# Optimization experiments

Measured on AMD Instinct MI355X. Metric: run time of the kernel, lower is better.

Reference implementation:

```python
import jax, jax.numpy as jnp
import numpy as np

D_MODEL = 2048
NUM_HEADS = 16
HEAD_DIM = D_MODEL // NUM_HEADS
D_FF = 4 * D_MODEL
B, L = 2, 2048
LN_EPS = 1e-6


def layer_norm(x, scale, bias):
    x32 = x.astype(jnp.float32)
    mu = jnp.mean(x32, axis=-1, keepdims=True)
    var = jnp.mean(jnp.square(x32 - mu), axis=-1, keepdims=True)
    return (x32 - mu) * jax.lax.rsqrt(var + LN_EPS) * scale + bias


def setup_inputs() -> dict:
    key = jax.random.key(0)
    ks = jax.random.split(key, 10)
    s = 1.0 / np.sqrt(D_MODEL)
    x = jax.random.normal(ks[0], (B, L, D_MODEL), dtype=jnp.float32)
    mask = jnp.tril(jnp.ones((L, L), dtype=bool))[None, None, :, :]  # causal [1,1,L,L]
    wq = jax.random.normal(ks[1], (D_MODEL, D_MODEL), jnp.float32) * s
    wk = jax.random.normal(ks[2], (D_MODEL, D_MODEL), jnp.float32) * s
    wv = jax.random.normal(ks[3], (D_MODEL, D_MODEL), jnp.float32) * s
    wo = jax.random.normal(ks[4], (D_MODEL, D_MODEL), jnp.float32) * s
    w1 = jax.random.normal(ks[5], (D_MODEL, D_FF), jnp.float32) * s
    b1 = jnp.zeros((D_FF,), jnp.float32)
    w2 = jax.random.normal(ks[6], (D_FF, D_MODEL), jnp.float32) * (1.0 / np.sqrt(D_FF))
    b2 = jnp.zeros((D_MODEL,), jnp.float32)
    ln1_scale = jnp.ones((D_MODEL,), jnp.float32)
    ln1_bias = jnp.zeros((D_MODEL,), jnp.float32)
    ln2_scale = jnp.ones((D_MODEL,), jnp.float32)
    ln2_bias = jnp.zeros((D_MODEL,), jnp.float32)
    return {"x": x, "mask": mask, "ln1_scale": ln1_scale, "ln1_bias": ln1_bias,
            "wq": wq, "wk": wk, "wv": wv, "wo": wo,
            "ln2_scale": ln2_scale, "ln2_bias": ln2_bias,
            "w1": w1, "b1": b1, "w2": w2, "b2": b2}


def reference(x, mask, ln1_scale, ln1_bias, wq, wk, wv, wo,
              ln2_scale, ln2_bias, w1, b1, w2, b2):
    residual = x
    h = layer_norm(x, ln1_scale, ln1_bias)
    b, l, _ = h.shape
    q = (h @ wq).reshape(b, l, NUM_HEADS, HEAD_DIM)
    k = (h @ wk).reshape(b, l, NUM_HEADS, HEAD_DIM)
    v = (h @ wv).reshape(b, l, NUM_HEADS, HEAD_DIM)
    scores = jnp.einsum('bqhd,bkhd->bhqk', q, k) / jnp.sqrt(jnp.float32(HEAD_DIM))
    scores = jnp.where(mask, scores, -100000.0)
    attn = jax.nn.softmax(scores, axis=-1)
    attn_out = jnp.einsum('bhqk,bkhd->bqhd', attn, v).reshape(b, l, D_MODEL)
    x = residual + attn_out @ wo
    mlp = jax.nn.gelu(layer_norm(x, ln2_scale, ln2_bias) @ w1 + b1)
    return x + mlp @ w2 + b2
```

## Files before the change

kernel.cpp:

```cpp
#include <hip/hip_runtime.h>
#include <hip/hip_bf16.h>

typedef unsigned short u16;
typedef __bf16 bf16x8 __attribute__((ext_vector_type(8)));
typedef float f32x4 __attribute__((ext_vector_type(4)));

#define D_MODEL 2048
#define D_FF    8192
#define NH      16
#define HD      128
#define BATCH   2
#define SEQ     2048
#define ROWS    (BATCH*SEQ)

__device__ __forceinline__ u16 f2bf(float f) {
  union { __hip_bfloat16 h; u16 u; } cv;
  cv.h = __float2bfloat16(f);
  return cv.u;
}

__device__ __forceinline__ void gload16(const u16* g, u16* l) {
  __builtin_amdgcn_global_load_lds((const __attribute__((address_space(1))) void*)g,
                                   (__attribute__((address_space(3))) void*)l,
                                   16, 0, 0);
}

__device__ __forceinline__ float gelu_f(float x) {
  const float k0 = 0.7978845608028654f, k1 = 0.044715f;
  return 0.5f * x * (1.0f + tanhf(k0 * (x + k1 * x * x * x)));
}

__global__ __launch_bounds__(256) void ln_bf16_kernel(
    const float* __restrict__ x, const float* __restrict__ sc,
    const float* __restrict__ bs, u16* __restrict__ out)
{
  __shared__ float red[8];
  const int row = blockIdx.x, t = threadIdx.x;
  const int w = t >> 6, l = t & 63;
  const float* xr = x + (size_t)row * D_MODEL;
  float4 a = ((const float4*)xr)[t*2];
  float4 b = ((const float4*)xr)[t*2+1];
  float s  = a.x+a.y+a.z+a.w + b.x+b.y+b.z+b.w;
  float s2 = a.x*a.x+a.y*a.y+a.z*a.z+a.w*a.w + b.x*b.x+b.y*b.y+b.z*b.z+b.w*b.w;
  for (int off = 32; off; off >>= 1) { s += __shfl_down(s, off); s2 += __shfl_down(s2, off); }
  if (l == 0) { red[w] = s; red[4+w] = s2; }
  __syncthreads();
  s  = red[0]+red[1]+red[2]+red[3];
  s2 = red[4]+red[5]+red[6]+red[7];
  const float mu  = s * (1.0f / D_MODEL);
  const float var = s2 * (1.0f / D_MODEL) - mu * mu;
  const float inv = rsqrtf(var + 1e-6f);
  float4 g0 = ((const float4*)sc)[t*2], g1 = ((const float4*)sc)[t*2+1];
  float4 q0 = ((const float4*)bs)[t*2], q1 = ((const float4*)bs)[t*2+1];
  union { u16 u[8]; uint4 v; } o;
  o.u[0] = f2bf((a.x-mu)*inv*g0.x + q0.x);
  o.u[1] = f2bf((a.y-mu)*inv*g0.y + q0.y);
  o.u[2] = f2bf((a.z-mu)*inv*g0.z + q0.z);
  o.u[3] = f2bf((a.w-mu)*inv*g0.w + q0.w);
  o.u[4] = f2bf((b.x-mu)*inv*g1.x + q1.x);
  o.u[5] = f2bf((b.y-mu)*inv*g1.y + q1.y);
  o.u[6] = f2bf((b.z-mu)*inv*g1.z + q1.z);
  o.u[7] = f2bf((b.w-mu)*inv*g1.w + q1.w);
  *(uint4*)(&out[(size_t)row * D_MODEL + t*8]) = o.v;
}

__global__ __launch_bounds__(256) void transpose_w(
    const float* __restrict__ in, u16* __restrict__ out, int R, int C)
{
  __shared__ float tile[32][33];
  const int t = threadIdx.x;
  const int c0 = blockIdx.x*32, r0 = blockIdx.y*32;
  const int col = t & 31, rb = t >> 5;
#pragma unroll
  for (int i = 0; i < 4; ++i)
    tile[rb + i*8][col] = in[(size_t)(r0 + rb + i*8)*C + c0 + col];
  __syncthreads();
#pragma unroll
  for (int i = 0; i < 4; ++i)
    out[(size_t)(c0 + rb + i*8)*R + r0 + col] = f2bf(tile[col][rb + i*8]);
}

__global__ __launch_bounds__(256) void transpose_v(
    const u16* __restrict__ qkv, u16* __restrict__ vt)
{
  __shared__ u16 tile[32][34];
  const int t = threadIdx.x;
  const int b = blockIdx.z;
  const int c0 = blockIdx.x*32, r0 = blockIdx.y*32;
  const int col = t & 31, rb = t >> 5;
  const u16* inb = qkv + (size_t)b*SEQ*3*D_MODEL + 2*D_MODEL;
#pragma unroll
  for (int i = 0; i < 4; ++i)
    tile[rb+i*8][col] = inb[(size_t)(r0+rb+i*8)*(3*D_MODEL) + c0+col];
  __syncthreads();
  u16* ob = vt + (size_t)b*SEQ*D_MODEL;
#pragma unroll
  for (int i = 0; i < 4; ++i)
    ob[(size_t)(c0+rb+i*8)*SEQ + r0+col] = tile[col][rb+i*8];
}

template<int EPI, int BNP>
__global__ __launch_bounds__(512, 1) void gemm8p(
    const u16* __restrict__ A, const u16* __restrict__ BT,
    void* __restrict__ Cout, const float* __restrict__ bias,
    const float* __restrict__ res, int N, int K, int gridN)
{
  constexpr int GB    = BNP / 128;
  constexpr int MF    = (BNP == 256) ? 8 : 4;
  constexpr int BHALF = BNP * 32;
  constexpr int BUFU  = 16384 + BNP * 64;
  __shared__ __align__(16) u16 lds[2 * BUFU];
  const int t = threadIdx.x;
  const int nwg = gridDim.x;
  const int wg = (int)blockIdx.x;
  const int wgid = (wg & 7) * (nwg >> 3) + (wg >> 3);
  const int bx = wgid % gridN, by = wgid / gridN;
  const int m0 = by * 256, n0 = bx * BNP;
  const int w = t >> 6, l = t & 63;
  const int wm = (BNP == 256) ? (w >> 2) : (w >> 1);
  const int wn = (BNP == 256) ? (w & 3) : (w & 1);
  const int l15 = l & 15, lq = l >> 4;

  const int srow = t >> 2;
  const int c0s  = (t & 3) ^ ((srow >> 1) & 3);
  const u16* aS0 = A  + (size_t)(m0 + srow) * K + c0s * 8;
  const u16* aS1 = A  + (size_t)(m0 + 128 + srow) * K + c0s * 8;
  const u16* bS0 = BT + (size_t)(n0 + srow) * K + c0s * 8;
  const u16* bS1 = BT + (size_t)(n0 + (GB == 2 ? 128 : 0) + srow) * K + c0s * 8;

  int offA_[MF], offB_[4];
#pragma unroll
  for (int i = 0; i < MF; ++i) {
    const int ra = wm * (MF * 16) + i * 16 + l15;
    offA_[i] = ra * 32 + ((lq ^ ((ra >> 1) & 3)) * 8);
  }
#pragma unroll
  for (int j = 0; j < 4; ++j) {
    const int rb = wn * 64 + j * 16 + l15;
    offB_[j] = rb * 32 + ((lq ^ ((rb >> 1) & 3)) * 8);
  }

  f32x4 acc[MF][4] = {};
  const int nt = K >> 6;

#define STAGE(dst, Tn, kh) { \
    gload16(aS0 + (size_t)(Tn)*64 + (kh)*32, (dst) + (kh)*8192 + t*8); \
    gload16(aS1 + (size_t)(Tn)*64 + (kh)*32, (dst) + (kh)*8192 + 4096 + t*8); \
    gload16(bS0 + (size_t)(Tn)*64 + (kh)*32, (dst) + 16384 + (kh)*BHALF + t*8); \
    if (GB == 2) gload16(bS1 + (size_t)(Tn)*64 + (kh)*32, (dst) + 16384 + (kh)*BHALF + 4096 + t*8); }
#define VMS { if (GB == 2) { asm volatile("s_waitcnt vmcnt(4)" ::: "memory"); } \
              else        { asm volatile("s_waitcnt vmcnt(3)" ::: "memory"); } \
              __builtin_amdgcn_sched_barrier(0); }
#define VM0 { asm volatile("s_waitcnt vmcnt(0)" ::: "memory"); __builtin_amdgcn_sched_barrier(0); }
#define NOP { }

#define PHASE(bufc, KH, STAGECODE, WAITCODE) { \
    bf16x8 af_[MF], bfv[4]; \
    _Pragma("unroll") \
    for (int i = 0; i < MF; ++i) \
      af_[i] = *(const bf16x8*)&(bufc)[offA_[i] + (KH)*8192]; \
    _Pragma("unroll") \
    for (int j = 0; j < 4; ++j) \
      bfv[j] = *(const bf16x8*)&(bufc)[offB_[j] + 16384 + (KH)*BHALF]; \
    STAGECODE; \
    __builtin_amdgcn_s_barrier(); \
    asm volatile("s_waitcnt lgkmcnt(0)" ::: "memory"); \
    __builtin_amdgcn_sched_barrier(0); \
    __builtin_amdgcn_s_setprio(1); \
    _Pragma("unroll") \
    for (int i = 0; i < MF; ++i) \
      _Pragma("unroll") \
      for (int j = 0; j < 4; ++j) \
        acc[i][j] = __builtin_amdgcn_mfma_f32_16x16x32_bf16(af_[i], bfv[j], acc[i][j], 0, 0, 0); \
    __builtin_amdgcn_s_setprio(0); \
    WAITCODE; \
    __builtin_amdgcn_s_barrier(); }

  STAGE(lds, 0, 0); STAGE(lds, 0, 1);
  VMS;
  __builtin_amdgcn_s_barrier();

  for (int T = 0; T < nt - 1; ++T) {
    u16* bufc = &lds[(T & 1) * BUFU];
    u16* bufn = &lds[((T + 1) & 1) * BUFU];
    PHASE(bufc, 0, STAGE(bufn, T + 1, 0), VMS);
    PHASE(bufc, 1, STAGE(bufn, T + 1, 1), VMS);
  }
  {
    u16* bufc = &lds[((nt - 1) & 1) * BUFU];
    PHASE(bufc, 0, NOP, VM0);
    PHASE(bufc, 1, NOP, NOP);
  }
#undef PHASE
#undef STAGE
#undef VMS
#undef VM0
#undef NOP

  const int rowb = m0 + wm * (MF * 16);
  const int colb = n0 + wn * 64;
#pragma unroll
  for (int mi = 0; mi < MF; ++mi) {
#pragma unroll
    for (int ni = 0; ni < 4; ++ni) {
      const int col = colb + ni * 16 + l15;
      const int row0 = rowb + mi * 16 + lq * 4;
      float bv = (EPI == 2 || EPI == 3) ? bias[col] : 0.f;
#pragma unroll
      for (int r = 0; r < 4; ++r) {
        const float v = acc[mi][ni][r];
        const size_t idx = (size_t)(row0 + r) * N + col;
        if (EPI == 0)      ((u16*)Cout)[idx] = f2bf(v);
        else if (EPI == 1) ((float*)Cout)[idx] = v + res[idx];
        else if (EPI == 2) ((u16*)Cout)[idx] = f2bf(gelu_f(v + bv));
        else               ((float*)Cout)[idx] = v + bv + res[idx];
      }
    }
  }
}

__global__ __launch_bounds__(256) void attn_kernel(
    const u16* __restrict__ qkv, const u16* __restrict__ vt,
    u16* __restrict__ out)
{
  __shared__ u16 Ks[64*128];
  __shared__ u16 Vs[128*64];
  __shared__ u16 Ps[4*16*64];
  const int t = threadIdx.x;
  const int pairi = blockIdx.x & 15, bh = blockIdx.x >> 4;
  const int b = bh >> 4, h = bh & 15;
  const int w = t >> 6, l = t & 63;
  const int l15 = l & 15, lq = l >> 4;
  const size_t kbase = (size_t)b*SEQ*(3*D_MODEL) + D_MODEL + h*HD;
  const size_t vbase = (size_t)(b*SEQ + h*HD) * SEQ;
  u16* pw = &Ps[w*1024];

  for (int qsel = 0; qsel < 2; ++qsel) {
    const int qt = qsel ? (31 - pairi) : pairi;

    bf16x8 qf[4];
    {
      const u16* qb = qkv + (size_t)(b*SEQ + qt*64 + w*16 + l15)*(3*D_MODEL) + h*HD;
#pragma unroll
      for (int kk = 0; kk < 4; ++kk)
        qf[kk] = *(const bf16x8*)(qb + kk*32 + lq*8);
    }
    float m[4]    = {-INFINITY, -INFINITY, -INFINITY, -INFINITY};
    float lsum[4] = {0.f, 0.f, 0.f, 0.f};
    f32x4 acc_o[8] = {};

    for (int j = 0; j <= qt; ++j) {
      __syncthreads();
#pragma unroll
      for (int i = 0; i < 4; ++i) {
        const int o16 = i*256 + t;
        {
          const int row = o16 >> 4, cs = o16 & 15;
          const int srcc = cs ^ (row & 7);
          gload16(qkv + kbase + (size_t)(j*64+row)*(3*D_MODEL) + srcc*8, &Ks[o16*8]);
        }
        {
          const int row = o16 >> 3, cs = o16 & 7;
          const int srcc = cs ^ (row & 7);
          gload16(vt + vbase + (size_t)row*SEQ + j*64 + srcc*8, &Vs[o16*8]);
        }
      }
      __syncthreads();

      f32x4 sacc[4] = {};
#pragma unroll
      for (int nf = 0; nf < 4; ++nf) {
        const int kr = nf*16 + l15;
        const int sw = kr & 7;
#pragma unroll
        for (int kk = 0; kk < 4; ++kk) {
          bf16x8 kf = *(const bf16x8*)&Ks[kr*128 + ((kk*4+lq) ^ sw)*8];
          sacc[nf] = __builtin_amdgcn_mfma_f32_16x16x32_bf16(qf[kk], kf, sacc[nf], 0, 0, 0);
        }
      }

      const float scale = 0.08838834764831845f;
      if (j == qt) {
#pragma unroll
        for (int nf = 0; nf < 4; ++nf)
#pragma unroll
          for (int r = 0; r < 4; ++r) {
            float s = sacc[nf][r] * scale;
            const int ki = nf*16 + l15;
            const int qi = w*16 + lq*4 + r;
            if (ki > qi) s = -100000.0f;
            sacc[nf][r] = s;
          }
      } else {
#pragma unroll
        for (int nf = 0; nf < 4; ++nf)
#pragma unroll
          for (int r = 0; r < 4; ++r) sacc[nf][r] *= scale;
      }

      float scal[4];
#pragma unroll
      for (int r = 0; r < 4; ++r) {
        float mx = fmaxf(fmaxf(sacc[0][r], sacc[1][r]), fmaxf(sacc[2][r], sacc[3][r]));
#pragma unroll
        for (int off = 1; off < 16; off <<= 1)
          mx = fmaxf(mx, __shfl_xor(mx, off));
        const float mn = fmaxf(m[r], mx);
        scal[r] = __expf(m[r] - mn);
        m[r] = mn;
        float rs = 0.f;
#pragma unroll
        for (int nf = 0; nf < 4; ++nf) {
          const float p = __expf(sacc[nf][r] - mn);
          sacc[nf][r] = p;
          rs += p;
        }
#pragma unroll
        for (int off = 1; off < 16; off <<= 1)
          rs += __shfl_xor(rs, off);
        lsum[r] = lsum[r]*scal[r] + rs;
      }
#pragma unroll
      for (int nf2 = 0; nf2 < 8; ++nf2)
#pragma unroll
        for (int r = 0; r < 4; ++r) acc_o[nf2][r] *= scal[r];

#pragma unroll
      for (int nf = 0; nf < 4; ++nf)
#pragma unroll
        for (int r = 0; r < 4; ++r) {
          const int qr = lq*4 + r, kc = nf*16 + l15;
          pw[qr*64 + (((kc>>3) ^ (qr&7))*8 + (kc&7))] = f2bf(sacc[nf][r]);
        }

#pragma unroll
      for (int kk2 = 0; kk2 < 2; ++kk2) {
        bf16x8 pf = *(const bf16x8*)&pw[l15*64 + (((kk2*4+lq) ^ (l15&7))*8)];
#pragma unroll
        for (int nf2 = 0; nf2 < 8; ++nf2) {
          const int vr = nf2*16 + l15;
          bf16x8 vf = *(const bf16x8*)&Vs[vr*64 + ((kk2*4+lq) ^ (vr&7))*8];
          acc_o[nf2] = __builtin_amdgcn_mfma_f32_16x16x32_bf16(pf, vf, acc_o[nf2], 0, 0, 0);
        }
      }
    }

    const size_t ro = (size_t)(b*SEQ + qt*64 + w*16 + lq*4);
#pragma unroll
    for (int r = 0; r < 4; ++r) {
      const float inv = 1.0f / lsum[r];
#pragma unroll
      for (int nf2 = 0; nf2 < 8; ++nf2)
        out[(ro + r)*D_MODEL + h*HD + nf2*16 + l15] = f2bf(acc_o[nf2][r] * inv);
    }
    __syncthreads();
  }
}

extern "C" void kernel_launch(void* const* d_in, const int* in_sizes, int n_in,
                              void* d_out, int out_size, void* d_ws, size_t ws_size,
                              hipStream_t stream)
{
  (void)in_sizes; (void)n_in; (void)out_size; (void)ws_size;
  const float* x    = (const float*)d_in[0];
  const float* ln1s = (const float*)d_in[2];
  const float* ln1b = (const float*)d_in[3];
  const float* wq   = (const float*)d_in[4];
  const float* wk   = (const float*)d_in[5];
  const float* wv   = (const float*)d_in[6];
  const float* wo   = (const float*)d_in[7];
  const float* ln2s = (const float*)d_in[8];
  const float* ln2b = (const float*)d_in[9];
  const float* w1   = (const float*)d_in[10];
  const float* b1   = (const float*)d_in[11];
  const float* w2   = (const float*)d_in[12];
  const float* b2   = (const float*)d_in[13];
  float* out = (float*)d_out;

  char* ws = (char*)d_ws;
  constexpr size_t OFF_WQKV = 0;
  constexpr size_t OFF_WO   = OFF_WQKV + (size_t)3*D_MODEL*D_MODEL*2;
  constexpr size_t OFF_W1   = OFF_WO   + (size_t)D_MODEL*D_MODEL*2;
  constexpr size_t OFF_W2   = OFF_W1   + (size_t)D_FF*D_MODEL*2;
  constexpr size_t OFF_H    = OFF_W2   + (size_t)D_MODEL*D_FF*2;
  constexpr size_t OFF_QKV  = OFF_H    + (size_t)ROWS*D_MODEL*2;
  constexpr size_t OFF_VT   = OFF_QKV  + (size_t)ROWS*3*D_MODEL*2;
  constexpr size_t OFF_ATTN = OFF_VT   + (size_t)ROWS*D_MODEL*2;
  constexpr size_t OFF_X2   = OFF_ATTN + (size_t)ROWS*D_MODEL*2;

  u16*   wqkv_bt = (u16*)(ws + OFF_WQKV);
  u16*   wo_bt   = (u16*)(ws + OFF_WO);
  u16*   w1_bt   = (u16*)(ws + OFF_W1);
  u16*   w2_bt   = (u16*)(ws + OFF_W2);
  u16*   h_bf    = (u16*)(ws + OFF_H);
  u16*   qkv     = (u16*)(ws + OFF_QKV);
  u16*   vt      = (u16*)(ws + OFF_VT);
  u16*   act     = qkv;
  u16*   attn    = (u16*)(ws + OFF_ATTN);
  float* x2      = (float*)(ws + OFF_X2);

  const dim3 B256(256), B512(512);

  transpose_w<<<dim3(64,64),  B256, 0, stream>>>(wq, wqkv_bt,                 D_MODEL, D_MODEL);
  transpose_w<<<dim3(64,64),  B256, 0, stream>>>(wk, wqkv_bt + (size_t)D_MODEL*D_MODEL,   D_MODEL, D_MODEL);
  transpose_w<<<dim3(64,64),  B256, 0, stream>>>(wv, wqkv_bt + (size_t)2*D_MODEL*D_MODEL, D_MODEL, D_MODEL);
  transpose_w<<<dim3(64,64),  B256, 0, stream>>>(wo, wo_bt, D_MODEL, D_MODEL);
  transpose_w<<<dim3(256,64), B256, 0, stream>>>(w1, w1_bt, D_MODEL, D_FF);
  transpose_w<<<dim3(64,256), B256, 0, stream>>>(w2, w2_bt, D_FF, D_MODEL);

  ln_bf16_kernel<<<ROWS, B256, 0, stream>>>(x, ln1s, ln1b, h_bf);
  gemm8p<0,128><<<dim3(768), B512, 0, stream>>>(h_bf, wqkv_bt, qkv, nullptr, nullptr, 3*D_MODEL, D_MODEL, 48);
  transpose_v<<<dim3(64,64,2), B256, 0, stream>>>(qkv, vt);
  attn_kernel<<<dim3(BATCH*NH*16), B256, 0, stream>>>(qkv, vt, attn);
  gemm8p<1,128><<<dim3(256), B512, 0, stream>>>(attn, wo_bt, (void*)x2, nullptr, x, D_MODEL, D_MODEL, 16);
  ln_bf16_kernel<<<ROWS, B256, 0, stream>>>(x2, ln2s, ln2b, h_bf);
  gemm8p<2,256><<<dim3(512), B512, 0, stream>>>(h_bf, w1_bt, act, b1, nullptr, D_FF, D_MODEL, 32);
  gemm8p<3,128><<<dim3(256), B512, 0, stream>>>(act, w2_bt, (void*)out, b2, x2, D_MODEL, D_FF, 16);
}
```

Before: 671.8 us.

## Replace double-buffered GEMM with triple-buffered 128x256 tile pipeline

Replaces the double-buffered GEMM with a triple-buffered variant that prefetches two K-tiles ahead and waits on fewer outstanding loads per step. All four projection GEMMs now use one 128x256 output tile instead of 256x128 or 256x256, and grids are adjusted to match. This aims to hide global-memory latency better. In exchange it uses more LDS and changes per-block reuse: FF1 loses its larger 256x256 tile and now needs twice as many blocks.

```diff
diff --git a/kernel.cpp b/kernel.cpp
--- a/kernel.cpp
+++ b/kernel.cpp
@@ -99,76 +99,72 @@
     ob[(size_t)(c0+rb+i*8)*SEQ + r0+col] = tile[col][rb+i*8];
 }
 
-template<int EPI, int BNP>
-__global__ __launch_bounds__(512, 1) void gemm8p(
+template<int EPI>
+__global__ __launch_bounds__(512, 1) void gemm_s3(
     const u16* __restrict__ A, const u16* __restrict__ BT,
     void* __restrict__ Cout, const float* __restrict__ bias,
     const float* __restrict__ res, int N, int K, int gridN)
 {
-  constexpr int GB    = BNP / 128;
-  constexpr int MF    = (BNP == 256) ? 8 : 4;
-  constexpr int BHALF = BNP * 32;
-  constexpr int BUFU  = 16384 + BNP * 64;
-  __shared__ __align__(16) u16 lds[2 * BUFU];
+  constexpr int BUFU = 24576;
+  __shared__ __align__(16) u16 lds[3 * BUFU];
   const int t = threadIdx.x;
   const int nwg = gridDim.x;
   const int wg = (int)blockIdx.x;
   const int wgid = (wg & 7) * (nwg >> 3) + (wg >> 3);
   const int bx = wgid % gridN, by = wgid / gridN;
-  const int m0 = by * 256, n0 = bx * BNP;
+  const int m0 = by * 128, n0 = bx * 256;
   const int w = t >> 6, l = t & 63;
-  const int wm = (BNP == 256) ? (w >> 2) : (w >> 1);
-  const int wn = (BNP == 256) ? (w & 3) : (w & 1);
+  const int wm = w >> 2, wn = w & 3;
   const int l15 = l & 15, lq = l >> 4;
 
-  const int srow = t >> 2;
-  const int c0s  = (t & 3) ^ ((srow >> 1) & 3);
-  const u16* aS0 = A  + (size_t)(m0 + srow) * K + c0s * 8;
-  const u16* aS1 = A  + (size_t)(m0 + 128 + srow) * K + c0s * 8;
-  const u16* bS0 = BT + (size_t)(n0 + srow) * K + c0s * 8;
-  const u16* bS1 = BT + (size_t)(n0 + (GB == 2 ? 128 : 0) + srow) * K + c0s * 8;
-
-  int offA_[MF], offB_[4];
-#pragma unroll
-  for (int i = 0; i < MF; ++i) {
-    const int ra = wm * (MF * 16) + i * 16 + l15;
-    offA_[i] = ra * 32 + ((lq ^ ((ra >> 1) & 3)) * 8);
+  const int arow = t >> 2,        achk = t & 3;
+  const int acs  = achk ^ ((arow >> 1) & 3);
+  const u16* aS  = A + (size_t)(m0 + arow) * K + acs * 8;
+  const int brow0 = t >> 2,        bchk0 = t & 3;
+  const int bcs0  = bchk0 ^ ((brow0 >> 1) & 3);
+  const u16* bS0  = BT + (size_t)(n0 + brow0) * K + bcs0 * 8;
+  const int brow1 = (512 + t) >> 2, bchk1 = t & 3;
+  const int bcs1  = bchk1 ^ ((brow1 >> 1) & 3);
+  const u16* bS1  = BT + (size_t)(n0 + brow1) * K + bcs1 * 8;
+
+  int offA_[2][4], offB_[2][4];
+#pragma unroll
+  for (int kh = 0; kh < 2; ++kh) {
+#pragma unroll
+    for (int i = 0; i < 4; ++i) {
+      const int ra = wm * 64 + i * 16 + l15;
+      offA_[kh][i] = kh * 4096 + ra * 32 + ((lq ^ ((ra >> 1) & 3)) * 8);
+      const int rb = wn * 64 + i * 16 + l15;
+      offB_[kh][i] = 8192 + kh * 8192 + rb * 32 + ((lq ^ ((rb >> 1) & 3)) * 8);
+    }
   }
-#pragma unroll
-  for (int j = 0; j < 4; ++j) {
-    const int rb = wn * 64 + j * 16 + l15;
-    offB_[j] = rb * 32 + ((lq ^ ((rb >> 1) & 3)) * 8);
-  }
-
-  f32x4 acc[MF][4] = {};
+
+  f32x4 acc[4][4] = {};
   const int nt = K >> 6;
 
-#define STAGE(dst, Tn, kh) { \
-    gload16(aS0 + (size_t)(Tn)*64 + (kh)*32, (dst) + (kh)*8192 + t*8); \
-    gload16(aS1 + (size_t)(Tn)*64 + (kh)*32, (dst) + (kh)*8192 + 4096 + t*8); \
-    gload16(bS0 + (size_t)(Tn)*64 + (kh)*32, (dst) + 16384 + (kh)*BHALF + t*8); \
-    if (GB == 2) gload16(bS1 + (size_t)(Tn)*64 + (kh)*32, (dst) + 16384 + (kh)*BHALF + 4096 + t*8); }
-#define VMS { if (GB == 2) { asm volatile("s_waitcnt vmcnt(4)" ::: "memory"); } \
-              else        { asm volatile("s_waitcnt vmcnt(3)" ::: "memory"); } \
-              __builtin_amdgcn_sched_barrier(0); }
+#define STAGEKH(Tn, bidx, kh) { u16* d = &lds[(bidx) * BUFU]; \
+    gload16(aS  + (size_t)(Tn)*64 + (kh)*32, d + (kh)*4096 + t*8); \
+    gload16(bS0 + (size_t)(Tn)*64 + (kh)*32, d + 8192 + (kh)*8192 + t*8); \
+    gload16(bS1 + (size_t)(Tn)*64 + (kh)*32, d + 8192 + (kh)*8192 + 4096 + t*8); }
+#define VM6 { asm volatile("s_waitcnt vmcnt(6)" ::: "memory"); __builtin_amdgcn_sched_barrier(0); }
 #define VM0 { asm volatile("s_waitcnt vmcnt(0)" ::: "memory"); __builtin_amdgcn_sched_barrier(0); }
-#define NOP { }
+#define NOPC { }
 
 #define PHASE(bufc, KH, STAGECODE, WAITCODE) { \
-    bf16x8 af_[MF], bfv[4]; \
+    bf16x8 af_[4], bfv[4]; \
     _Pragma("unroll") \
-    for (int i = 0; i < MF; ++i) \
-      af_[i] = *(const bf16x8*)&(bufc)[offA_[i] + (KH)*8192]; \
+    for (int i = 0; i < 4; ++i) \
+      af_[i] = *(const bf16x8*)&(bufc)[offA_[KH][i]]; \
     _Pragma("unroll") \
     for (int j = 0; j < 4; ++j) \
-      bfv[j] = *(const bf16x8*)&(bufc)[offB_[j] + 16384 + (KH)*BHALF]; \
+      bfv[j] = *(const bf16x8*)&(bufc)[offB_[KH][j]]; \
     STAGECODE; \
     __builtin_amdgcn_s_barrier(); \
     asm volatile("s_waitcnt lgkmcnt(0)" ::: "memory"); \
     __builtin_amdgcn_sched_barrier(0); \
     __builtin_amdgcn_s_setprio(1); \
     _Pragma("unroll") \
-    for (int i = 0; i < MF; ++i) \
+    for (int i = 0; i < 4; ++i) \
       _Pragma("unroll") \
       for (int j = 0; j < 4; ++j) \
         acc[i][j] = __builtin_amdgcn_mfma_f32_16x16x32_bf16(af_[i], bfv[j], acc[i][j], 0, 0, 0); \
@@ -176,31 +172,37 @@
     WAITCODE; \
     __builtin_amdgcn_s_barrier(); }
 
-  STAGE(lds, 0, 0); STAGE(lds, 0, 1);
-  VMS;
+  STAGEKH(0, 0, 0); STAGEKH(0, 0, 1); STAGEKH(1, 1, 0); STAGEKH(1, 1, 1);
+  VM6;
   __builtin_amdgcn_s_barrier();
 
-  for (int T = 0; T < nt - 1; ++T) {
-    u16* bufc = &lds[(T & 1) * BUFU];
-    u16* bufn = &lds[((T + 1) & 1) * BUFU];
-    PHASE(bufc, 0, STAGE(bufn, T + 1, 0), VMS);
-    PHASE(bufc, 1, STAGE(bufn, T + 1, 1), VMS);
+  int cur = 0;
+  for (int T = 0; T < nt - 2; ++T) {
+    u16* bufc = &lds[cur * BUFU];
+    const int stg = (cur == 0) ? 2 : cur - 1;
+    PHASE(bufc, 0, STAGEKH(T + 2, stg, 0), NOPC);
+    PHASE(bufc, 1, STAGEKH(T + 2, stg, 1), VM6);
+    cur = (cur == 2) ? 0 : cur + 1;
   }
   {
-    u16* bufc = &lds[((nt - 1) & 1) * BUFU];
-    PHASE(bufc, 0, NOP, VM0);
-    PHASE(bufc, 1, NOP, NOP);
+    u16* bufc = &lds[cur * BUFU];
+    PHASE(bufc, 0, NOPC, NOPC);
+    PHASE(bufc, 1, NOPC, VM0);
+    cur = (cur == 2) ? 0 : cur + 1;
+    u16* bufl = &lds[cur * BUFU];
+    PHASE(bufl, 0, NOPC, NOPC);
+    PHASE(bufl, 1, NOPC, NOPC);
   }
 #undef PHASE
-#undef STAGE
-#undef VMS
+#undef STAGEKH
+#undef VM6
 #undef VM0
-#undef NOP
-
-  const int rowb = m0 + wm * (MF * 16);
+#undef NOPC
+
+  const int rowb = m0 + wm * 64;
   const int colb = n0 + wn * 64;
 #pragma unroll
-  for (int mi = 0; mi < MF; ++mi) {
+  for (int mi = 0; mi < 4; ++mi) {
 #pragma unroll
     for (int ni = 0; ni < 4; ++ni) {
       const int col = colb + ni * 16 + l15;
@@ -409,11 +411,11 @@
   transpose_w<<<dim3(64,256), B256, 0, stream>>>(w2, w2_bt, D_FF, D_MODEL);
 
   ln_bf16_kernel<<<ROWS, B256, 0, stream>>>(x, ln1s, ln1b, h_bf);
-  gemm8p<0,128><<<dim3(768), B512, 0, stream>>>(h_bf, wqkv_bt, qkv, nullptr, nullptr, 3*D_MODEL, D_MODEL, 48);
+  gemm_s3<0><<<dim3(768), B512, 0, stream>>>(h_bf, wqkv_bt, qkv, nullptr, nullptr, 3*D_MODEL, D_MODEL, 24);
   transpose_v<<<dim3(64,64,2), B256, 0, stream>>>(qkv, vt);
   attn_kernel<<<dim3(BATCH*NH*16), B256, 0, stream>>>(qkv, vt, attn);
-  gemm8p<1,128><<<dim3(256), B512, 0, stream>>>(attn, wo_bt, (void*)x2, nullptr, x, D_MODEL, D_MODEL, 16);
+  gemm_s3<1><<<dim3(256), B512, 0, stream>>>(attn, wo_bt, (void*)x2, nullptr, x, D_MODEL, D_MODEL, 8);
   ln_bf16_kernel<<<ROWS, B256, 0, stream>>>(x2, ln2s, ln2b, h_bf);
-  gemm8p<2,256><<<dim3(512), B512, 0, stream>>>(h_bf, w1_bt, act, b1, nullptr, D_FF, D_MODEL, 32);
-  gemm8p<3,128><<<dim3(256), B512, 0, stream>>>(act, w2_bt, (void*)out, b2, x2, D_MODEL, D_FF, 16);
-}
+  gemm_s3<2><<<dim3(1024), B512, 0, stream>>>(h_bf, w1_bt, act, b1, nullptr, D_FF, D_MODEL, 32);
+  gemm_s3<3><<<dim3(256), B512, 0, stream>>>(act, w2_bt, (void*)out, b2, x2, D_MODEL, D_FF, 8);
+}
```

Result: slower. 725.0 us (+7.9%).
